# Kernel optimization log

Measured on AMD Instinct MI355X. Metric: run time of the kernel, lower is better.

Reference implementation:

```python
import jax, jax.numpy as jnp
import numpy as np
import math

B, N, D, H = 32, 577, 768, 12
HD = D // H  # 64
WS = 24  # window size
NUM_REL_DIST = (2 * WS - 1) * (2 * WS - 1) + 3  # 2212


def _build_rel_pos_index():
    ch, cw = np.arange(WS), np.arange(WS)
    coords = np.stack(np.meshgrid(ch, cw, indexing='ij'))  # [2, WS, WS]
    cf = coords.reshape(2, -1)  # [2, WS*WS]
    rel = cf[:, :, None] - cf[:, None, :]  # [2, WS*WS, WS*WS]
    rel = rel.transpose(1, 2, 0).astype(np.int64)
    rel[:, :, 0] += WS - 1
    rel[:, :, 1] += WS - 1
    rel[:, :, 0] *= 2 * WS - 1
    idx = np.zeros((WS * WS + 1, WS * WS + 1), dtype=np.int64)
    idx[1:, 1:] = rel.sum(-1)
    idx[0, 0:] = NUM_REL_DIST - 3
    idx[0:, 0] = NUM_REL_DIST - 2
    idx[0, 0] = NUM_REL_DIST - 1
    return idx.astype(np.int32)


def setup_inputs() -> dict:
    key = jax.random.key(0)
    ks = jax.random.split(key, 7)
    s = 1.0 / math.sqrt(D)
    return {
        'hidden_states': jax.random.normal(ks[0], (B, N, D), jnp.float32),
        'q_w': jax.random.normal(ks[1], (D, D), jnp.float32) * s,
        'q_b': jax.random.normal(ks[2], (D,), jnp.float32) * 0.02,
        'k_w': jax.random.normal(ks[3], (D, D), jnp.float32) * s,
        'v_w': jax.random.normal(ks[4], (D, D), jnp.float32) * s,
        'v_b': jax.random.normal(ks[5], (D,), jnp.float32) * 0.02,
        'rel_pos_table': jax.random.normal(ks[6], (NUM_REL_DIST, H), jnp.float32) * 0.02,
        'rel_pos_index': jnp.asarray(_build_rel_pos_index()),
    }


def reference(hidden_states, q_w, q_b, k_w, v_w, v_b, rel_pos_table, rel_pos_index):
    # QKV projections (torch Linear: x @ W.T + b); key has no bias
    q = hidden_states @ q_w.T + q_b  # [B,N,D]
    k = hidden_states @ k_w.T        # [B,N,D]
    v = hidden_states @ v_w.T + v_b  # [B,N,D]

    def heads(x):
        return x.reshape(B, N, H, HD).transpose(0, 2, 1, 3)  # [B,H,N,HD]

    q, k, v = heads(q), heads(k), heads(v)
    scores = jnp.einsum('bhqd,bhkd->bhqk', q, k) / math.sqrt(HD)
    # relative position bias: table lookup -> [N,N,H] -> [H,N,N]
    bias = rel_pos_table[rel_pos_index.reshape(-1)].reshape(N, N, H)
    scores = scores + bias.transpose(2, 0, 1)[None]
    probs = jax.nn.softmax(scores, axis=-1)  # dropout p=0 (eval)
    ctx = jnp.einsum('bhqk,bhkd->bhqd', probs, v)
    return ctx.transpose(0, 2, 1, 3).reshape(B, N, D)
```

## Files before the change

### kernel.cpp

```cpp
#include <hip/hip_runtime.h>
#include <hip/hip_bf16.h>

#define B_  32
#define N_  577
#define D_  768
#define H_  12
#define HD_ 64
#define M_  (B_ * N_)
#define NW_ (3 * D_)
#define VN_ 640
#define BPAD_ 640
#define SCALE_ 0.18033688f

typedef __bf16 bf16_t;
typedef __bf16 bf16x8 __attribute__((ext_vector_type(8)));
typedef __bf16 bf16x4 __attribute__((ext_vector_type(4)));
typedef float  f32x4  __attribute__((ext_vector_type(4)));

static __device__ __forceinline__ bf16x8 ldg8(const bf16_t* p) {
    return *reinterpret_cast<const bf16x8*>(p);
}

#define GLOAD_LDS16(g, l)                                                     \
    __builtin_amdgcn_global_load_lds(                                         \
        (const __attribute__((address_space(1))) void*)(g),                   \
        (__attribute__((address_space(3))) void*)(l), 16, 0, 0)

__global__ void cvt_f32_bf16(const float* __restrict__ src,
                             bf16_t* __restrict__ dst, int n4) {
    int i = blockIdx.x * blockDim.x + threadIdx.x;
    if (i < n4) {
        float4 f = reinterpret_cast<const float4*>(src)[i];
        bf16x4 o;
        o.x = (bf16_t)f.x; o.y = (bf16_t)f.y; o.z = (bf16_t)f.z; o.w = (bf16_t)f.w;
        *reinterpret_cast<bf16x4*>(dst + (size_t)i * 4) = o;
    }
}

__global__ void cvt3_f32_bf16(const float* __restrict__ s0,
                              const float* __restrict__ s1,
                              const float* __restrict__ s2,
                              bf16_t* __restrict__ dst, int n4) {
    int i = blockIdx.x * blockDim.x + threadIdx.x;
    if (i < n4) {
        const float* src = blockIdx.y == 0 ? s0 : (blockIdx.y == 1 ? s1 : s2);
        float4 f = reinterpret_cast<const float4*>(src)[i];
        bf16x4 o;
        o.x = (bf16_t)f.x; o.y = (bf16_t)f.y; o.z = (bf16_t)f.z; o.w = (bf16_t)f.w;
        *reinterpret_cast<bf16x4*>(dst + (size_t)blockIdx.y * n4 * 4 + (size_t)i * 4) = o;
    }
}

__global__ void build_bias_t(const float* __restrict__ table,
                             const int* __restrict__ idx,
                             float* __restrict__ biasT) {
    int col = blockIdx.x;
    int h   = blockIdx.y;
    float* dst = biasT + ((size_t)h * BPAD_ + col) * BPAD_;
    if (col < N_) {
        for (int row = threadIdx.x; row < BPAD_; row += blockDim.x) {
            int rr = row < N_ ? row : (N_ - 1);
            int id = idx[rr * N_ + col];
            dst[row] = table[id * H_ + h] * 1.44269504f;
        }
    } else {
        for (int row = threadIdx.x; row < BPAD_; row += blockDim.x)
            dst[row] = -1e30f;
    }
}

__global__ __launch_bounds__(256) void qkv_gemm(
    const bf16_t* __restrict__ hb, const bf16_t* __restrict__ W,
    const float* __restrict__ qb, const float* __restrict__ vb,
    bf16_t* __restrict__ Q, bf16_t* __restrict__ K, bf16_t* __restrict__ VT)
{
    __shared__ __align__(16) char lds[65536];

    int tid = threadIdx.x;
    int w  = tid >> 6, l = tid & 63;
    int lr = l & 15, lg = l >> 4;
    int wm = w & 1,  wn = w >> 1;

    int wg = blockIdx.x;
    int xcd = wg & 7, pos = wg >> 3;
    const int Q8 = 2610 / 8, R8 = 2610 % 8;
    int base = xcd < R8 ? xcd * (Q8 + 1) : R8 * (Q8 + 1) + (xcd - R8) * Q8;
    int wgid = base + pos;
    int bx = wgid / 18, y = wgid - bx * 18;
    int brow = bx * 128;
    int mat = y / 6, ysub = y - mat * 6;
    int cbase = ysub * 128;

    int srow = tid >> 3;
    int sslot = (tid & 7) ^ (srow & 7);
    const bf16_t* pa[4];
    const bf16_t* pb[4];
#pragma unroll
    for (int r = 0; r < 4; ++r) {
        int ra = brow + r * 32 + srow; ra = ra < M_ ? ra : (M_ - 1);
        pa[r] = hb + (size_t)ra * D_ + sslot * 8;
        pb[r] = W + (size_t)(y * 128 + r * 32 + srow) * D_ + sslot * 8;
    }

    auto stage = [&](int buf, int k) {
#pragma unroll
        for (int r = 0; r < 4; ++r) {
            GLOAD_LDS16(pa[r] + k, lds + buf * 16384 + r * 4096 + tid * 16);
            GLOAD_LDS16(pb[r] + k, lds + 32768 + buf * 16384 + r * 4096 + tid * 16);
        }
    };

    f32x4 acc[4][4] = {};
    stage(0, 0);
    int cur = 0;
    for (int t = 0; t < 12; ++t) {
        if (t < 11) {
            stage(cur ^ 1, (t + 1) * 64);
            asm volatile("s_waitcnt vmcnt(8)" ::: "memory");
        } else {
            asm volatile("s_waitcnt vmcnt(0)" ::: "memory");
        }
        __builtin_amdgcn_s_barrier();
        __builtin_amdgcn_sched_barrier(0);

        const char* pA = lds + cur * 16384;
        const char* pB = lds + 32768 + cur * 16384;
#pragma unroll
        for (int kk = 0; kk < 2; ++kk) {
            bf16x8 af[4];
#pragma unroll
            for (int m = 0; m < 4; ++m) {
                int row = wm * 64 + m * 16 + lr;
                af[m] = *reinterpret_cast<const bf16x8*>(
                    pA + row * 128 + (((kk * 4 + lg) ^ (lr & 7)) << 4));
            }
#pragma unroll
            for (int n = 0; n < 4; ++n) {
                int row = wn * 64 + n * 16 + lr;
                bf16x8 bfr = *reinterpret_cast<const bf16x8*>(
                    pB + row * 128 + (((kk * 4 + lg) ^ (lr & 7)) << 4));
#pragma unroll
                for (int m = 0; m < 4; ++m)
                    acc[m][n] = __builtin_amdgcn_mfma_f32_16x16x32_bf16(
                        af[m], bfr, acc[m][n], 0, 0, 0);
            }
        }
        __builtin_amdgcn_sched_barrier(0);
        __builtin_amdgcn_s_barrier();
        cur ^= 1;
    }

    bf16_t* ep = (bf16_t*)lds;
    if (mat < 2) {
#pragma unroll
        for (int m = 0; m < 4; ++m)
#pragma unroll
            for (int n = 0; n < 4; ++n) {
                int col = wn * 64 + n * 16 + lr;
#pragma unroll
                for (int j = 0; j < 4; ++j) {
                    int row = wm * 64 + m * 16 + lg * 4 + j;
                    float v = acc[m][n][j];
                    v = (mat == 0) ? (v + qb[cbase + col]) * SCALE_ : v;
                    ep[row * 132 + col] = (bf16_t)v;
                }
            }
        __syncthreads();
        bf16_t* dst0 = (mat == 0) ? Q : K;
#pragma unroll
        for (int k = 0; k < 8; ++k) {
            int c = k * 256 + tid;
            int row = c >> 4, cc = c & 15;
            int grow = brow + row;
            if (grow < M_) {
                int bb = grow / N_, nn = grow - bb * N_;
                int col0 = cc * 8;
                int hh = ysub * 2 + (col0 >> 6);
                int hd0 = col0 & 63;
                bf16x8 vc = *reinterpret_cast<const bf16x8*>(ep + row * 132 + col0);
                *reinterpret_cast<bf16x8*>(
                    dst0 + ((size_t)(bb * H_ + hh) * N_ + nn) * HD_ + hd0) = vc;
            }
        }
    } else {
#pragma unroll
        for (int m = 0; m < 4; ++m)
#pragma unroll
            for (int n = 0; n < 4; ++n) {
                int col = wn * 64 + n * 16 + lr;
                float badd = vb[cbase + col];
#pragma unroll
                for (int j = 0; j < 4; ++j) {
                    int row = wm * 64 + m * 16 + lg * 4 + j;
                    ep[col * 132 + row] = (bf16_t)(acc[m][n][j] + badd);
                }
            }
        __syncthreads();
#pragma unroll
        for (int k = 0; k < 8; ++k) {
            int c = k * 256 + tid;
            int col = c >> 4, rc = c & 15;
            int grow0 = brow + rc * 8;
            int hh = ysub * 2 + (col >> 6), hd = col & 63;
            int bb = grow0 / N_, nn0 = grow0 - bb * N_;
            if (nn0 + 8 <= N_ && grow0 + 8 <= M_) {
                *reinterpret_cast<bf16x8*>(
                    VT + ((size_t)(bb * H_ + hh) * HD_ + hd) * VN_ + nn0) =
                    *reinterpret_cast<const bf16x8*>(ep + col * 132 + rc * 8);
            } else {
                for (int jj = 0; jj < 8; ++jj) {
                    int grow = grow0 + jj;
                    if (grow >= M_) break;
                    int b2 = grow / N_, n2 = grow - b2 * N_;
                    VT[((size_t)(b2 * H_ + hh) * HD_ + hd) * VN_ + n2] =
                        ep[col * 132 + rc * 8 + jj];
                }
            }
        }
    }
}

__global__ __launch_bounds__(256) void attn(
    const bf16_t* __restrict__ Q, const bf16_t* __restrict__ K,
    const bf16_t* __restrict__ VT, const float* __restrict__ biasT,
    float* __restrict__ out)
{
    __shared__ __align__(16) char Kl[2][8192];
    __shared__ __align__(16) char Vl[8192];
    __shared__ __align__(16) char Pl[4][2048];

    int tid = threadIdx.x;
    int w = tid >> 6, l = tid & 63, lr = l & 15, lg = l >> 4;

    int wg = blockIdx.x;
    int wgid = (wg & 7) * 480 + (wg >> 3);
    int h = wgid / 320;
    int rem = wgid - h * 320;
    int b = rem / 10;
    int qt = rem - b * 10;

    const bf16_t* Qp = Q  + (size_t)(b * H_ + h) * N_ * HD_;
    const bf16_t* Kp = K  + (size_t)(b * H_ + h) * N_ * HD_;
    const bf16_t* Vp = VT + (size_t)(b * H_ + h) * HD_ * VN_;
    const float*  bp = biasT + (size_t)h * BPAD_ * BPAD_;

    int q0 = qt * 64 + w * 16;
    int qrow = q0 + lr;
    int qrow_c = qrow < N_ ? qrow : (N_ - 1);
    bf16x8 aQ0 = ldg8(Qp + (size_t)qrow_c * HD_ + lg * 8);
    bf16x8 aQ1 = ldg8(Qp + (size_t)qrow_c * HD_ + 32 + lg * 8);

    bf16x8 vone;
#pragma unroll
    for (int i = 0; i < 8; ++i) vone[i] = (bf16_t)1.0f;

    int rloc = l >> 3;
    int cswz = (l & 7) ^ rloc;
    const bf16_t* Kst[2];
    const bf16_t* Vst[2];
#pragma unroll
    for (int rnd = 0; rnd < 2; ++rnd) {
        int r = rnd * 32 + w * 8 + rloc;
        Kst[rnd] = Kp + (size_t)r * HD_ + cswz * 8;
        Vst[rnd] = Vp + (size_t)r * VN_ + cswz * 8;
    }

    f32x4 o[4] = {};
    f32x4 osum = {};
    char* Pw = Pl[w];

#pragma unroll
    for (int rnd = 0; rnd < 2; ++rnd)
        GLOAD_LDS16(Kst[rnd], Kl[0] + rnd * 4096 + w * 1024);
    __syncthreads();

    int cur = 0;
    const int NT = 10;
    for (int t = 0; t < NT; ++t) {
        int k0 = t * 64;

#pragma unroll
        for (int rnd = 0; rnd < 2; ++rnd)
            GLOAD_LDS16(Vst[rnd] + k0, Vl + rnd * 4096 + w * 1024);
        f32x4 bb[4];
#pragma unroll
        for (int kt = 0; kt < 4; ++kt) {
            bb[kt] = *reinterpret_cast<const f32x4*>(
                bp + (size_t)(k0 + kt * 16 + lr) * BPAD_ + q0 + lg * 4);
        }
        __builtin_amdgcn_sched_barrier(0);
        if (t + 1 < NT) {
#pragma unroll
            for (int rnd = 0; rnd < 2; ++rnd)
                GLOAD_LDS16(Kst[rnd] + (size_t)(k0 + 64) * HD_,
                            Kl[cur ^ 1] + rnd * 4096 + w * 1024);
        }
        __builtin_amdgcn_sched_barrier(0);

        f32x4 s[4];
        __builtin_amdgcn_s_setprio(1);
#pragma unroll
        for (int kt = 0; kt < 4; ++kt) {
            int r = kt * 16 + lr;
            bf16x8 kf0 = *reinterpret_cast<const bf16x8*>(
                Kl[cur] + r * 128 + ((lg ^ (r & 7)) << 4));
            bf16x8 kf1 = *reinterpret_cast<const bf16x8*>(
                Kl[cur] + r * 128 + (((4 + lg) ^ (r & 7)) << 4));
            f32x4 a = __builtin_amdgcn_mfma_f32_16x16x32_bf16(aQ0, kf0, bb[kt], 0, 0, 0);
            s[kt] = __builtin_amdgcn_mfma_f32_16x16x32_bf16(aQ1, kf1, a, 0, 0, 0);
        }
        __builtin_amdgcn_s_setprio(0);

#pragma unroll
        for (int kt = 0; kt < 4; ++kt)
#pragma unroll
            for (int j = 0; j < 4; ++j) {
                float p = __builtin_amdgcn_exp2f(s[kt][j]);
                int row = lg * 4 + j;
                int byte = (row * 128 + (kt * 16 + lr) * 2) ^ ((row & 7) << 4);
                *reinterpret_cast<bf16_t*>(Pw + byte) = (bf16_t)p;
            }

        if (t + 1 < NT) asm volatile("s_waitcnt vmcnt(2)" ::: "memory");
        else            asm volatile("s_waitcnt vmcnt(0)" ::: "memory");
        __builtin_amdgcn_s_barrier();
        __builtin_amdgcn_sched_barrier(0);

        __builtin_amdgcn_s_setprio(1);
#pragma unroll
        for (int kc = 0; kc < 2; ++kc) {
            int pbyte = (lr * 128 + kc * 64 + lg * 16) ^ ((lr & 7) << 4);
            bf16x8 aP = *reinterpret_cast<const bf16x8*>(Pw + pbyte);
            osum = __builtin_amdgcn_mfma_f32_16x16x32_bf16(aP, vone, osum, 0, 0, 0);
#pragma unroll
            for (int ft = 0; ft < 4; ++ft) {
                int d = ft * 16 + lr;
                bf16x8 bV = *reinterpret_cast<const bf16x8*>(
                    Vl + d * 128 + (((kc * 4 + lg) ^ (d & 7)) << 4));
                o[ft] = __builtin_amdgcn_mfma_f32_16x16x32_bf16(aP, bV, o[ft], 0, 0, 0);
            }
        }
        __builtin_amdgcn_s_setprio(0);
        __builtin_amdgcn_sched_barrier(0);

        asm volatile("s_waitcnt vmcnt(0)" ::: "memory");
        __builtin_amdgcn_s_barrier();
        __builtin_amdgcn_sched_barrier(0);
        cur ^= 1;
    }

#pragma unroll
    for (int j = 0; j < 4; ++j) {
        int row = q0 + lg * 4 + j;
        if (row < N_) {
            float inv = 1.f / osum[j];
#pragma unroll
            for (int ft = 0; ft < 4; ++ft)
                out[((size_t)(b * N_ + row)) * D_ + h * HD_ + ft * 16 + lr] =
                    o[ft][j] * inv;
        }
    }
}

extern "C" void kernel_launch(void* const* d_in, const int* in_sizes, int n_in,
                              void* d_out, int out_size, void* d_ws, size_t ws_size,
                              hipStream_t stream)
{
    const float* hs    = (const float*)d_in[0];
    const float* q_w   = (const float*)d_in[1];
    const float* q_b   = (const float*)d_in[2];
    const float* k_w   = (const float*)d_in[3];
    const float* v_w   = (const float*)d_in[4];
    const float* v_b   = (const float*)d_in[5];
    const float* table = (const float*)d_in[6];
    const int*   rpi   = (const int*)d_in[7];
    float* out = (float*)d_out;

    char* ws = (char*)d_ws;
    size_t off = 0;
    auto alloc = [&](size_t bytes) {
        char* p = ws + off;
        off = (off + bytes + 255) & ~(size_t)255;
        return p;
    };
    bf16_t* hb  = (bf16_t*)alloc((size_t)M_ * D_ * 2);
    bf16_t* Wc  = (bf16_t*)alloc((size_t)NW_ * D_ * 2);
    bf16_t* Qb  = (bf16_t*)alloc((size_t)B_ * H_ * N_ * HD_ * 2);
    bf16_t* Kb  = (bf16_t*)alloc((size_t)B_ * H_ * N_ * HD_ * 2 + 8192);
    bf16_t* VTb = (bf16_t*)alloc((size_t)B_ * H_ * HD_ * VN_ * 2);
    float*  bia = (float*)alloc((size_t)H_ * BPAD_ * BPAD_ * 4);

    int n4h = M_ * D_ / 4;
    cvt_f32_bf16<<<(n4h + 255) / 256, 256, 0, stream>>>(hs, hb, n4h);
    int n4w = D_ * D_ / 4;
    cvt3_f32_bf16<<<dim3((n4w + 255) / 256, 3), 256, 0, stream>>>(
        q_w, k_w, v_w, Wc, n4w);
    build_bias_t<<<dim3(BPAD_, H_), 256, 0, stream>>>(table, rpi, bia);

    qkv_gemm<<<2610, 256, 0, stream>>>(hb, Wc, q_b, v_b, Qb, Kb, VTb);

    attn<<<3840, 256, 0, stream>>>(Qb, Kb, VTb, bia, out);
}
```

Measured before the change: 240.5 us.

## Double-buffer V and prefetch bias one tile ahead in attention loop

```diff
diff --git a/kernel.cpp b/kernel.cpp
--- a/kernel.cpp
+++ b/kernel.cpp
@@ -226,7 +226,7 @@
     float* __restrict__ out)
 {
     __shared__ __align__(16) char Kl[2][8192];
-    __shared__ __align__(16) char Vl[8192];
+    __shared__ __align__(16) char Vl[2][8192];
     __shared__ __align__(16) char Pl[4][2048];
 
     int tid = threadIdx.x;
@@ -268,32 +268,29 @@
     f32x4 o[4] = {};
     f32x4 osum = {};
     char* Pw = Pl[w];
-
-#pragma unroll
-    for (int rnd = 0; rnd < 2; ++rnd)
-        GLOAD_LDS16(Kst[rnd], Kl[0] + rnd * 4096 + w * 1024);
-    __syncthreads();
-
-    int cur = 0;
     const int NT = 10;
-    for (int t = 0; t < NT; ++t) {
+
+    auto stageKV = [&](int buf, int k0) {
+#pragma unroll
+        for (int rnd = 0; rnd < 2; ++rnd)
+            GLOAD_LDS16(Kst[rnd] + (size_t)k0 * HD_,
+                        Kl[buf] + rnd * 4096 + w * 1024);
+#pragma unroll
+        for (int rnd = 0; rnd < 2; ++rnd)
+            GLOAD_LDS16(Vst[rnd] + k0, Vl[buf] + rnd * 4096 + w * 1024);
+    };
+    auto loadBias = [&](int k0, f32x4* bbv) {
+#pragma unroll
+        for (int kt = 0; kt < 4; ++kt)
+            bbv[kt] = *reinterpret_cast<const f32x4*>(
+                bp + (size_t)(k0 + kt * 16 + lr) * BPAD_ + q0 + lg * 4);
+    };
+
+    auto tile = [&](int t, int rbuf, const f32x4* bbcur, f32x4* bbnxt) {
         int k0 = t * 64;
-
-#pragma unroll
-        for (int rnd = 0; rnd < 2; ++rnd)
-            GLOAD_LDS16(Vst[rnd] + k0, Vl + rnd * 4096 + w * 1024);
-        f32x4 bb[4];
-#pragma unroll
-        for (int kt = 0; kt < 4; ++kt) {
-            bb[kt] = *reinterpret_cast<const f32x4*>(
-                bp + (size_t)(k0 + kt * 16 + lr) * BPAD_ + q0 + lg * 4);
-        }
-        __builtin_amdgcn_sched_barrier(0);
         if (t + 1 < NT) {
-#pragma unroll
-            for (int rnd = 0; rnd < 2; ++rnd)
-                GLOAD_LDS16(Kst[rnd] + (size_t)(k0 + 64) * HD_,
-                            Kl[cur ^ 1] + rnd * 4096 + w * 1024);
+            stageKV(rbuf ^ 1, k0 + 64);
+            loadBias(k0 + 64, bbnxt);
         }
         __builtin_amdgcn_sched_barrier(0);
 
@@ -303,10 +300,11 @@
         for (int kt = 0; kt < 4; ++kt) {
             int r = kt * 16 + lr;
             bf16x8 kf0 = *reinterpret_cast<const bf16x8*>(
-                Kl[cur] + r * 128 + ((lg ^ (r & 7)) << 4));
+                Kl[rbuf] + r * 128 + ((lg ^ (r & 7)) << 4));
             bf16x8 kf1 = *reinterpret_cast<const bf16x8*>(
-                Kl[cur] + r * 128 + (((4 + lg) ^ (r & 7)) << 4));
-            f32x4 a = __builtin_amdgcn_mfma_f32_16x16x32_bf16(aQ0, kf0, bb[kt], 0, 0, 0);
+                Kl[rbuf] + r * 128 + (((4 + lg) ^ (r & 7)) << 4));
+            f32x4 a = __builtin_amdgcn_mfma_f32_16x16x32_bf16(
+                aQ0, kf0, bbcur[kt], 0, 0, 0);
             s[kt] = __builtin_amdgcn_mfma_f32_16x16x32_bf16(aQ1, kf1, a, 0, 0, 0);
         }
         __builtin_amdgcn_s_setprio(0);
@@ -321,11 +319,6 @@
                 *reinterpret_cast<bf16_t*>(Pw + byte) = (bf16_t)p;
             }
 
-        if (t + 1 < NT) asm volatile("s_waitcnt vmcnt(2)" ::: "memory");
-        else            asm volatile("s_waitcnt vmcnt(0)" ::: "memory");
-        __builtin_amdgcn_s_barrier();
-        __builtin_amdgcn_sched_barrier(0);
-
         __builtin_amdgcn_s_setprio(1);
 #pragma unroll
         for (int kc = 0; kc < 2; ++kc) {
@@ -336,17 +329,29 @@
             for (int ft = 0; ft < 4; ++ft) {
                 int d = ft * 16 + lr;
                 bf16x8 bV = *reinterpret_cast<const bf16x8*>(
-                    Vl + d * 128 + (((kc * 4 + lg) ^ (d & 7)) << 4));
+                    Vl[rbuf] + d * 128 + (((kc * 4 + lg) ^ (d & 7)) << 4));
                 o[ft] = __builtin_amdgcn_mfma_f32_16x16x32_bf16(aP, bV, o[ft], 0, 0, 0);
             }
         }
         __builtin_amdgcn_s_setprio(0);
         __builtin_amdgcn_sched_barrier(0);
 
-        asm volatile("s_waitcnt vmcnt(0)" ::: "memory");
+        if (t + 1 < NT) asm volatile("s_waitcnt vmcnt(4)" ::: "memory");
+        else            asm volatile("s_waitcnt vmcnt(0)" ::: "memory");
         __builtin_amdgcn_s_barrier();
         __builtin_amdgcn_sched_barrier(0);
-        cur ^= 1;
+    };
+
+    f32x4 bbA[4], bbB[4];
+    stageKV(0, 0);
+    loadBias(0, bbA);
+    asm volatile("s_waitcnt vmcnt(4)" ::: "memory");
+    __builtin_amdgcn_s_barrier();
+    __builtin_amdgcn_sched_barrier(0);
+
+    for (int tp = 0; tp < NT / 2; ++tp) {
+        tile(tp * 2,     0, bbA, bbB);
+        tile(tp * 2 + 1, 1, bbB, bbA);
     }
 
 #pragma unroll
@@ -386,7 +391,7 @@
     bf16_t* hb  = (bf16_t*)alloc((size_t)M_ * D_ * 2);
     bf16_t* Wc  = (bf16_t*)alloc((size_t)NW_ * D_ * 2);
     bf16_t* Qb  = (bf16_t*)alloc((size_t)B_ * H_ * N_ * HD_ * 2);
-    bf16_t* Kb  = (bf16_t*)alloc((size_t)B_ * H_ * N_ * HD_ * 2 + 8192);
+    bf16_t* Kb  = (bf16_t*)alloc((size_t)B_ * H_ * N_ * HD_ * 2 + 16384);
     bf16_t* VTb = (bf16_t*)alloc((size_t)B_ * H_ * HD_ * VN_ * 2);
     float*  bia = (float*)alloc((size_t)H_ * BPAD_ * BPAD_ * 4);
 
```

Measured after the change: 238.4 us. No clear change (-0.9%).
